# Kernel tuning notes

Measured on AMD Instinct MI355X. Metric: run time of the kernel, lower is better.

## Reference

```python
import jax, jax.numpy as jnp
import numpy as np

# Dims: B=16 graphs, T=354 timesteps (l_max), N=64 nodes, H=128 model dim, NS=32 complex SSM modes

def setup_inputs() -> dict:
    key = jax.random.key(0)
    ks = jax.random.split(key, 10)
    B, T, N, H, NS = 16, 354, 64, 128, 32
    x = jax.random.normal(ks[0], (B, T, N), jnp.float32)
    W_in = jax.random.normal(ks[1], (H, 1), jnp.float32) * 0.5
    b_in = jnp.zeros((H,), jnp.float32)
    # S4D params: timescales log-uniform in [1e-3, 1e-1], A = -1/2 + i*pi*n (S4D-Lin init)
    log_dt = (jnp.log(0.001) + jax.random.uniform(ks[2], (H,), jnp.float32) * (jnp.log(0.1) - jnp.log(0.001))).astype(jnp.float32)
    A_re = -0.5 * jnp.ones((H, NS), jnp.float32)
    A_im = jnp.broadcast_to(np.pi * jnp.arange(NS, dtype=jnp.float32), (H, NS)).astype(jnp.float32) + 0.0
    C_re = jax.random.normal(ks[3], (H, NS), jnp.float32) * (0.5 ** 0.5)
    C_im = jax.random.normal(ks[4], (H, NS), jnp.float32) * (0.5 ** 0.5)
    D = jax.random.normal(ks[5], (H,), jnp.float32)
    W_out = jax.random.normal(ks[6], (2 * H, H), jnp.float32) * (1.0 / np.sqrt(H))
    b_out = jnp.zeros((2 * H,), jnp.float32)
    W_cls = jax.random.normal(ks[7], (1, H), jnp.float32) * (1.0 / np.sqrt(H))
    b_cls = jnp.zeros((1,), jnp.float32)
    return {"x": x, "W_in": W_in, "b_in": b_in, "log_dt": log_dt, "A_re": A_re, "A_im": A_im,
            "C_re": C_re, "C_im": C_im, "D": D, "W_out": W_out, "b_out": b_out,
            "W_cls": W_cls, "b_cls": b_cls}


def reference(x, W_in, b_in, log_dt, A_re, A_im, C_re, C_im, D, W_out, b_out, W_cls, b_cls):
    B, T, N = x.shape
    H = W_in.shape[0]
    # (B,T,N) -> (B*N, T, 1) per-node scalar series
    u = x.transpose(0, 2, 1).reshape(B * N, T, 1)
    u = u * W_in[:, 0] + b_in            # input_proj: (BN, T, H)
    u = u.transpose(0, 2, 1)             # transposed layout: (BN, H, L)
    # ---- S4D kernel (ZOH discretization, conjugate-pair 2*Re trick) ----
    dt = jnp.exp(log_dt)                 # (H,)
    A = A_re + 1j * A_im                 # (H, NS) complex64
    dtA = A * dt[:, None]                # (H, NS)
    C = C_re + 1j * C_im
    C_disc = C * (jnp.exp(dtA) - 1.0) / A
    l = jnp.arange(T)
    vand = jnp.exp(dtA[:, :, None] * l)  # Vandermonde (H, NS, L)
    K = 2.0 * jnp.real(jnp.einsum('hn,hnl->hl', C_disc, vand))  # (H, L)
    # ---- FFT causal long convolution + skip ----
    n_fft = 2 * T
    yf = jnp.fft.rfft(u, n_fft) * jnp.fft.rfft(K, n_fft)
    y = jnp.fft.irfft(yf, n_fft)[..., :T] + D[:, None] * u   # (BN, H, L)
    y = jax.nn.gelu(y)
    # dropout: identity at inference
    # ---- position-wise output linear H -> 2H, then GLU over channels ----
    g = jnp.einsum('bhl,gh->bgl', y, W_out) + b_out[:, None]  # (BN, 2H, L)
    z = g[:, :H] * jax.nn.sigmoid(g[:, H:])                    # (BN, H, L)
    # ---- pooling + classifier ----
    node_feats = z.mean(axis=-1).reshape(B, N, H)
    graph_feats = node_feats.mean(axis=1)                      # (B, H)
    logits = graph_feats @ W_cls.T + b_cls                     # (B, 1)
    return logits
```

## Files before the change

kernel.cpp:

```cpp
#include <hip/hip_runtime.h>
#include <hip/hip_bf16.h>


#define B_  16
#define T_  354
#define N_  64
#define H_  128
#define NS_ 32
#define BN_ (B_*N_)
#define TP_ 384
#define KW_ 512
#define TC_ 23

typedef __attribute__((ext_vector_type(8))) short bf16x8;
typedef __attribute__((ext_vector_type(4))) float f32x4;

static __device__ __forceinline__ unsigned short f32_to_bf16(float f) {
    unsigned int u = __float_as_uint(f);
    unsigned int r = 0x7FFFu + ((u >> 16) & 1u);
    return (unsigned short)((u + r) >> 16);
}

__global__ void k_wprep(const float* __restrict__ W_out, unsigned short* __restrict__ Wbf) {
    int i = blockIdx.x * blockDim.x + threadIdx.x;
    if (i < 2 * H_ * H_) Wbf[i] = f32_to_bf16(W_out[i]);
}

__global__ void k_xprep(const float* __restrict__ x, unsigned short* __restrict__ xbf) {
    int id = blockIdx.x * blockDim.x + threadIdx.x;
    if (id >= T_ * BN_) return;
    int t  = id >> 10;
    int bn = id & 1023;
    float v = x[(bn >> 6) * (T_ * N_) + t * N_ + (bn & 63)];
    xbf[bn * TP_ + t] = f32_to_bf16(v);
}

__global__ __launch_bounds__(512) void k_kern(
        const float* __restrict__ log_dt,
        const float* __restrict__ A_re, const float* __restrict__ A_im,
        const float* __restrict__ C_re, const float* __restrict__ C_im,
        const float* __restrict__ b_in, const float* __restrict__ D,
        unsigned short* __restrict__ Krev, float* __restrict__ koff) {
    const int h = blockIdx.x;
    const int l = threadIdx.x;

    float val = 0.0f;
    if (l < T_) {
        float dt = expf(log_dt[h]);
        float fl = (float)l;
#pragma unroll 4
        for (int m = 0; m < NS_; m++) {
            float are = A_re[h * NS_ + m], aim = A_im[h * NS_ + m];
            float dre = are * dt, dim = aim * dt;
            float er  = expf(dre);
            float c1, s1; __sincosf(dim, &s1, &c1);
            float e_re = er * c1, e_im = er * s1;
            float m_re = e_re - 1.0f, m_im = e_im;
            float inv  = 1.0f / (are * are + aim * aim);
            float q_re = (m_re * are + m_im * aim) * inv;
            float q_im = (m_im * are - m_re * aim) * inv;
            float c_r = C_re[h * NS_ + m], c_i = C_im[h * NS_ + m];
            float cdre = c_r * q_re - c_i * q_im;
            float cdim = c_r * q_im + c_i * q_re;
            float el = expf(dre * fl);
            float cl, sl; __sincosf(dim * fl, &sl, &cl);
            val += el * (cdre * cl - cdim * sl);
        }
        val *= 2.0f;
        if (l == 0) val += D[h];
    }

    __shared__ float sc[512];
    sc[l] = (l < T_) ? val : 0.0f;
    __syncthreads();
    for (int off = 1; off < 512; off <<= 1) {
        float add = (l >= off) ? sc[l - off] : 0.0f;
        __syncthreads();
        sc[l] += add;
        __syncthreads();
    }

    if (l < T_) {
        koff[l * H_ + h] = b_in[h] * sc[l];
        unsigned short bv = f32_to_bf16(val);
#pragma unroll
        for (int r = 0; r < 8; r++)
            Krev[((size_t)r * H_ + h) * KW_ + (T_ - 1 - l) + r] = bv;
    }
}

__global__ __launch_bounds__(256, 2) void k_conv(
        const unsigned short* __restrict__ xbf,
        const unsigned short* __restrict__ Krev,
        const float* __restrict__ koff,
        const float* __restrict__ W_in,
        unsigned short* __restrict__ Y) {
    const int tid  = threadIdx.x;
    const int w    = tid >> 6;
    const int lane = tid & 63;
    const int quad = lane >> 4;
    const int l16  = lane & 15;
    const int bn0  = blockIdx.x * 128;
    const int t    = blockIdx.y;
    const int h0   = w * 32;
    const int nkb  = (t >> 7) + 1;

    f32x4 acc[8][2];
#pragma unroll
    for (int mt = 0; mt < 8; mt++)
#pragma unroll
        for (int nt = 0; nt < 2; nt++) acc[mt][nt] = (f32x4){0.f, 0.f, 0.f, 0.f};

    for (int kb = 0; kb < nkb; kb++) {
        const int tau0 = kb << 7;
        const int s    = (T_ - 1) - t + tau0;
        const int r    = (-s) & 7;
        const unsigned short* bb = Krev + (size_t)r * H_ * KW_ + (s + r);

#pragma unroll
        for (int ks = 0; ks < 4; ks++) {
            bf16x8 bfr[2];
#pragma unroll
            for (int nt = 0; nt < 2; nt++)
                bfr[nt] = *(const bf16x8*)(bb + (h0 + nt * 16 + l16) * KW_
                                           + ks * 32 + quad * 8);
#pragma unroll
            for (int mt = 0; mt < 8; mt++) {
                bf16x8 afr = *(const bf16x8*)(xbf + (size_t)(bn0 + mt * 16 + l16) * TP_
                                              + tau0 + ks * 32 + quad * 8);
                acc[mt][0] = __builtin_amdgcn_mfma_f32_16x16x32_bf16(afr, bfr[0], acc[mt][0], 0, 0, 0);
                acc[mt][1] = __builtin_amdgcn_mfma_f32_16x16x32_bf16(afr, bfr[1], acc[mt][1], 0, 0, 0);
            }
        }
    }

    float win[2], ko[2];
#pragma unroll
    for (int nt = 0; nt < 2; nt++) {
        int h = h0 + nt * 16 + l16;
        win[nt] = W_in[h];
        ko[nt]  = koff[t * H_ + h];
    }

#pragma unroll
    for (int mt = 0; mt < 8; mt++)
#pragma unroll
        for (int nt = 0; nt < 2; nt++)
#pragma unroll
            for (int rr = 0; rr < 4; rr++) {
                float v = fmaf(acc[mt][nt][rr], win[nt], ko[nt]);
                float a  = 0.7978845608028654f * fmaf(0.044715f, v * v * v, v);
                float e  = __expf(2.0f * a);
                float th = 1.0f - 2.0f / (e + 1.0f);
                float g  = 0.5f * v * (1.0f + th);
                int bn = bn0 + mt * 16 + quad * 4 + rr;
                int h  = h0 + nt * 16 + l16;
                Y[((size_t)t * BN_ + bn) * H_ + h] = f32_to_bf16(g);
            }
}

__global__ __launch_bounds__(256, 2) void k_glu(
        const unsigned short* __restrict__ Ybf,
        const unsigned short* __restrict__ Wbf,
        const float* __restrict__ b_out,
        float* __restrict__ node_sum) {
    __shared__ unsigned short W_lds[128 * 136];

    const int tid  = threadIdx.x;
    const int w    = tid >> 6;
    const int lane = tid & 63;
    const int quad = lane >> 4;
    const int l16  = lane & 15;
    const int bn0  = blockIdx.x * 32;
    const int t0   = blockIdx.y * TC_;

    bf16x8 bfrag[4][4];

    for (int p = 0; p < 2; p++) {
        __syncthreads();
#pragma unroll
        for (int it = 0; it < 16; it++) {
            int c  = it * 256 + tid;
            int r  = c >> 5;
            int k4 = (c & 31) * 4;
            uint2 v = *(const uint2*)(Wbf + (size_t)(p * 128 + r) * 128 + k4);
            *(uint2*)&W_lds[r * 136 + k4] = v;
        }
        __syncthreads();
#pragma unroll
        for (int nt = 0; nt < 2; nt++) {
            int r = 32 * w + 16 * nt + l16;
#pragma unroll
            for (int ks = 0; ks < 4; ks++)
                bfrag[p * 2 + nt][ks] = *(const bf16x8*)&W_lds[r * 136 + ks * 32 + quad * 8];
        }
    }

    float bo1[2], bo2[2];
#pragma unroll
    for (int p = 0; p < 2; p++) {
        bo1[p] = b_out[32 * w + 16 * p + l16];
        bo2[p] = b_out[128 + 32 * w + 16 * p + l16];
    }

    f32x4 zacc[2][2];
#pragma unroll
    for (int mt = 0; mt < 2; mt++)
#pragma unroll
        for (int p = 0; p < 2; p++) zacc[mt][p] = (f32x4){0.f, 0.f, 0.f, 0.f};

    for (int tt = 0; tt < TC_; tt++) {
        int t = t0 + tt;
        if (t >= T_) break;
        const unsigned short* yrow = Ybf + (size_t)(t * BN_ + bn0) * H_;

        bf16x8 afrag[2][4];
#pragma unroll
        for (int mt = 0; mt < 2; mt++)
#pragma unroll
            for (int ks = 0; ks < 4; ks++)
                afrag[mt][ks] = *(const bf16x8*)(yrow + (size_t)(16 * mt + l16) * H_
                                                 + ks * 32 + quad * 8);

        f32x4 acc[2][4];
#pragma unroll
        for (int mt = 0; mt < 2; mt++)
#pragma unroll
            for (int nt = 0; nt < 4; nt++) acc[mt][nt] = (f32x4){0.f, 0.f, 0.f, 0.f};

#pragma unroll
        for (int ks = 0; ks < 4; ks++)
#pragma unroll
            for (int nt = 0; nt < 4; nt++)
#pragma unroll
                for (int mt = 0; mt < 2; mt++)
                    acc[mt][nt] = __builtin_amdgcn_mfma_f32_16x16x32_bf16(
                        afrag[mt][ks], bfrag[nt][ks], acc[mt][nt], 0, 0, 0);

#pragma unroll
        for (int mt = 0; mt < 2; mt++)
#pragma unroll
            for (int p = 0; p < 2; p++)
#pragma unroll
                for (int r = 0; r < 4; r++) {
                    float a  = acc[mt][p][r] + bo1[p];
                    float bs = acc[mt][p + 2][r] + bo2[p];
                    float sg = 1.0f / (1.0f + __expf(-bs));
                    zacc[mt][p][r] += a * sg;
                }
    }

#pragma unroll
    for (int mt = 0; mt < 2; mt++)
#pragma unroll
        for (int p = 0; p < 2; p++)
#pragma unroll
            for (int r = 0; r < 4; r++) {
                int bn = bn0 + 16 * mt + quad * 4 + r;
                int j  = 32 * w + 16 * p + l16;
                atomicAdd(&node_sum[bn * H_ + j], zacc[mt][p][r]);
            }
}

__global__ void k_cls(const float* __restrict__ node_sum,
                      const float* __restrict__ W_cls, const float* __restrict__ b_cls,
                      float* __restrict__ out) {
    const int b = blockIdx.x, tid = threadIdx.x;
    float s = 0.0f;
    for (int i = tid; i < N_ * H_; i += 256)
        s += node_sum[b * (N_ * H_) + i] * W_cls[i & (H_ - 1)];
    __shared__ float red[256];
    red[tid] = s;
    __syncthreads();
    for (int off = 128; off > 0; off >>= 1) {
        if (tid < off) red[tid] += red[tid + off];
        __syncthreads();
    }
    if (tid == 0) out[b] = red[0] * (1.0f / (354.0f * 64.0f)) + b_cls[0];
}

extern "C" void kernel_launch(void* const* d_in, const int* in_sizes, int n_in,
                              void* d_out, int out_size, void* d_ws, size_t ws_size,
                              hipStream_t stream) {
    const float* x      = (const float*)d_in[0];
    const float* W_in   = (const float*)d_in[1];
    const float* b_in   = (const float*)d_in[2];
    const float* log_dt = (const float*)d_in[3];
    const float* A_re   = (const float*)d_in[4];
    const float* A_im   = (const float*)d_in[5];
    const float* C_re   = (const float*)d_in[6];
    const float* C_im   = (const float*)d_in[7];
    const float* D      = (const float*)d_in[8];
    const float* W_out  = (const float*)d_in[9];
    const float* b_out  = (const float*)d_in[10];
    const float* W_cls  = (const float*)d_in[11];
    const float* b_cls  = (const float*)d_in[12];

    float* ws = (float*)d_ws;
    float*          node_sum = ws;
    float*          koff     = ws + 131072;
    unsigned short* Wbf      = (unsigned short*)(ws + 176384);
    unsigned short* xbf      = (unsigned short*)(ws + 192768);
    unsigned short* Krev     = (unsigned short*)(ws + 389376);
    unsigned short* Y        = (unsigned short*)(ws + 651520);

    hipMemsetAsync(node_sum, 0, (size_t)BN_ * H_ * sizeof(float), stream);
    hipMemsetAsync(xbf,  0, (size_t)BN_ * TP_ * 2, stream);
    hipMemsetAsync(Krev, 0, (size_t)8 * H_ * KW_ * 2, stream);

    k_wprep<<<dim3(2 * H_ * H_ / 256), dim3(256), 0, stream>>>(W_out, Wbf);
    k_xprep<<<dim3((T_ * BN_ + 255) / 256), dim3(256), 0, stream>>>(x, xbf);
    k_kern<<<dim3(H_), dim3(512), 0, stream>>>(
        log_dt, A_re, A_im, C_re, C_im, b_in, D, Krev, koff);
    k_conv<<<dim3(BN_ / 128, T_), dim3(256), 0, stream>>>(xbf, Krev, koff, W_in, Y);
    k_glu<<<dim3(BN_ / 32, (T_ + TC_ - 1) / TC_), dim3(256), 0, stream>>>(
        Y, Wbf, b_out, node_sum);
    k_cls<<<dim3(B_), dim3(256), 0, stream>>>(node_sum, W_cls, b_cls, (float*)d_out);
}
```

Baseline: 281.4 us.

## Retile causal conv as per-channel Toeplitz GEMM with LDS staging

The convolution kernel is restructured so each block handles one channel h and a 128x128 tile of (node, time). It stages the input rows and the shifted Toeplitz rows of the kernel into LDS with global_load_lds, then runs 4x4 MFMA tiles per wave, replacing the per-timestep grid that reloaded kernel fragments straight from global memory. The GLU kernel now stages each Y timestep tile through LDS, and its time chunk drops from 23 to 6 steps, which gives more blocks. The two prep kernels and the three memsets are merged into one kernel and one memset. In exchange, Y stores become strided by h, with one channel per lane, so write coalescing may get worse.

```diff
diff --git a/kernel.cpp b/kernel.cpp
--- a/kernel.cpp
+++ b/kernel.cpp
@@ -8,9 +8,10 @@
 #define H_  128
 #define NS_ 32
 #define BN_ (B_*N_)
+#define M_  (T_*BN_)
 #define TP_ 384
 #define KW_ 512
-#define TC_ 23
+#define TC_ 6
 
 typedef __attribute__((ext_vector_type(8))) short bf16x8;
 typedef __attribute__((ext_vector_type(4))) float f32x4;
@@ -21,18 +22,24 @@
     return (unsigned short)((u + r) >> 16);
 }
 
-__global__ void k_wprep(const float* __restrict__ W_out, unsigned short* __restrict__ Wbf) {
-    int i = blockIdx.x * blockDim.x + threadIdx.x;
-    if (i < 2 * H_ * H_) Wbf[i] = f32_to_bf16(W_out[i]);
-}
-
-__global__ void k_xprep(const float* __restrict__ x, unsigned short* __restrict__ xbf) {
+static __device__ __forceinline__ void gload_lds4(const void* g, void* l) {
+    __builtin_amdgcn_global_load_lds(
+        (const __attribute__((address_space(1))) unsigned int*)g,
+        (__attribute__((address_space(3))) unsigned int*)l, 4, 0, 0);
+}
+
+__global__ void k_prep(const float* __restrict__ x, const float* __restrict__ W_out,
+                       unsigned short* __restrict__ xbf, unsigned short* __restrict__ Wbf) {
     int id = blockIdx.x * blockDim.x + threadIdx.x;
-    if (id >= T_ * BN_) return;
-    int t  = id >> 10;
-    int bn = id & 1023;
-    float v = x[(bn >> 6) * (T_ * N_) + t * N_ + (bn & 63)];
-    xbf[bn * TP_ + t] = f32_to_bf16(v);
+    if (id < T_ * BN_) {
+        int t  = id >> 10;
+        int bn = id & 1023;
+        float v = x[(bn >> 6) * (T_ * N_) + t * N_ + (bn & 63)];
+        xbf[bn * TP_ + t] = f32_to_bf16(v);
+    } else {
+        int i = id - T_ * BN_;
+        if (i < 2 * H_ * H_) Wbf[i] = f32_to_bf16(W_out[i]);
+    }
 }
 
 __global__ __launch_bounds__(512) void k_kern(
@@ -95,68 +102,88 @@
         const float* __restrict__ koff,
         const float* __restrict__ W_in,
         unsigned short* __restrict__ Y) {
+    __shared__ unsigned short A_lds[128 * 136];
+    __shared__ unsigned short B_lds[128 * 136];
+
     const int tid  = threadIdx.x;
     const int w    = tid >> 6;
     const int lane = tid & 63;
     const int quad = lane >> 4;
     const int l16  = lane & 15;
-    const int bn0  = blockIdx.x * 128;
-    const int t    = blockIdx.y;
-    const int h0   = w * 32;
-    const int nkb  = (t >> 7) + 1;
-
-    f32x4 acc[8][2];
-#pragma unroll
-    for (int mt = 0; mt < 8; mt++)
-#pragma unroll
-        for (int nt = 0; nt < 2; nt++) acc[mt][nt] = (f32x4){0.f, 0.f, 0.f, 0.f};
+    const int h    = blockIdx.x;
+    const int bn0  = blockIdx.y * 128;
+    const int t0   = blockIdx.z * 128;
+    const int wm   = (w & 1) * 64;
+    const int wn   = (w >> 1) * 64;
+    const int nkb  = (t0 >> 7) + 1;
+
+    f32x4 acc[4][4];
+#pragma unroll
+    for (int mt = 0; mt < 4; mt++)
+#pragma unroll
+        for (int nt = 0; nt < 4; nt++) acc[mt][nt] = (f32x4){0.f, 0.f, 0.f, 0.f};
+
+    const unsigned short* krow = Krev + (size_t)h * KW_;
 
     for (int kb = 0; kb < nkb; kb++) {
         const int tau0 = kb << 7;
-        const int s    = (T_ - 1) - t + tau0;
-        const int r    = (-s) & 7;
-        const unsigned short* bb = Krev + (size_t)r * H_ * KW_ + (s + r);
+        __syncthreads();
+#pragma unroll 8
+        for (int i = 0; i < 32; i++) {
+            int r = w * 32 + i;
+            gload_lds4(xbf + (size_t)(bn0 + r) * TP_ + tau0 + lane * 2,
+                       &A_lds[r * 136]);
+        }
+#pragma unroll 8
+        for (int i = 0; i < 32; i++) {
+            int r = w * 32 + i;
+            int L = 353 - (t0 + r) + tau0;
+            if (L < 0) L = 0;
+            int cp = (-L) & 7;
+            gload_lds4(krow + (size_t)cp * H_ * KW_ + L + cp + lane * 2,
+                       &B_lds[r * 136]);
+        }
+        __syncthreads();
 
 #pragma unroll
         for (int ks = 0; ks < 4; ks++) {
-            bf16x8 bfr[2];
-#pragma unroll
-            for (int nt = 0; nt < 2; nt++)
-                bfr[nt] = *(const bf16x8*)(bb + (h0 + nt * 16 + l16) * KW_
-                                           + ks * 32 + quad * 8);
-#pragma unroll
-            for (int mt = 0; mt < 8; mt++) {
-                bf16x8 afr = *(const bf16x8*)(xbf + (size_t)(bn0 + mt * 16 + l16) * TP_
-                                              + tau0 + ks * 32 + quad * 8);
-                acc[mt][0] = __builtin_amdgcn_mfma_f32_16x16x32_bf16(afr, bfr[0], acc[mt][0], 0, 0, 0);
-                acc[mt][1] = __builtin_amdgcn_mfma_f32_16x16x32_bf16(afr, bfr[1], acc[mt][1], 0, 0, 0);
-            }
-        }
-    }
-
-    float win[2], ko[2];
-#pragma unroll
-    for (int nt = 0; nt < 2; nt++) {
-        int h = h0 + nt * 16 + l16;
-        win[nt] = W_in[h];
-        ko[nt]  = koff[t * H_ + h];
-    }
-
-#pragma unroll
-    for (int mt = 0; mt < 8; mt++)
-#pragma unroll
-        for (int nt = 0; nt < 2; nt++)
+            bf16x8 af[4], bfr[4];
+#pragma unroll
+            for (int mt = 0; mt < 4; mt++)
+                af[mt] = *(const bf16x8*)&A_lds[(wm + mt * 16 + l16) * 136 + ks * 32 + quad * 8];
+#pragma unroll
+            for (int nt = 0; nt < 4; nt++)
+                bfr[nt] = *(const bf16x8*)&B_lds[(wn + nt * 16 + l16) * 136 + ks * 32 + quad * 8];
+#pragma unroll
+            for (int nt = 0; nt < 4; nt++)
+#pragma unroll
+                for (int mt = 0; mt < 4; mt++)
+                    acc[mt][nt] = __builtin_amdgcn_mfma_f32_16x16x32_bf16(
+                        af[mt], bfr[nt], acc[mt][nt], 0, 0, 0);
+        }
+    }
+
+    const float win = W_in[h];
+#pragma unroll
+    for (int nt = 0; nt < 4; nt++) {
+        int t = t0 + wn + nt * 16 + l16;
+        bool ok  = (t < T_);
+        float ko = ok ? koff[t * H_ + h] : 0.0f;
+#pragma unroll
+        for (int mt = 0; mt < 4; mt++)
 #pragma unroll
             for (int rr = 0; rr < 4; rr++) {
-                float v = fmaf(acc[mt][nt][rr], win[nt], ko[nt]);
+                float v = fmaf(acc[mt][nt][rr], win, ko);
                 float a  = 0.7978845608028654f * fmaf(0.044715f, v * v * v, v);
                 float e  = __expf(2.0f * a);
                 float th = 1.0f - 2.0f / (e + 1.0f);
                 float g  = 0.5f * v * (1.0f + th);
-                int bn = bn0 + mt * 16 + quad * 4 + rr;
-                int h  = h0 + nt * 16 + l16;
-                Y[((size_t)t * BN_ + bn) * H_ + h] = f32_to_bf16(g);
+                if (ok) {
+                    int bn = bn0 + wm + mt * 16 + quad * 4 + rr;
+                    Y[((size_t)t * BN_ + bn) * H_ + h] = f32_to_bf16(g);
+                }
             }
+    }
 }
 
 __global__ __launch_bounds__(256, 2) void k_glu(
@@ -165,6 +192,7 @@
         const float* __restrict__ b_out,
         float* __restrict__ node_sum) {
     __shared__ unsigned short W_lds[128 * 136];
+    __shared__ unsigned short Yt[32 * 136];
 
     const int tid  = threadIdx.x;
     const int w    = tid >> 6;
@@ -212,15 +240,21 @@
     for (int tt = 0; tt < TC_; tt++) {
         int t = t0 + tt;
         if (t >= T_) break;
-        const unsigned short* yrow = Ybf + (size_t)(t * BN_ + bn0) * H_;
+        __syncthreads();
+#pragma unroll
+        for (int i = 0; i < 8; i++) {
+            int r = w * 8 + i;
+            gload_lds4(Ybf + ((size_t)t * BN_ + bn0 + r) * H_ + lane * 2,
+                       &Yt[r * 136]);
+        }
+        __syncthreads();
 
         bf16x8 afrag[2][4];
 #pragma unroll
         for (int mt = 0; mt < 2; mt++)
 #pragma unroll
             for (int ks = 0; ks < 4; ks++)
-                afrag[mt][ks] = *(const bf16x8*)(yrow + (size_t)(16 * mt + l16) * H_
-                                                 + ks * 32 + quad * 8);
+                afrag[mt][ks] = *(const bf16x8*)&Yt[(mt * 16 + l16) * 136 + ks * 32 + quad * 8];
 
         f32x4 acc[2][4];
 #pragma unroll
@@ -296,23 +330,20 @@
     const float* W_cls  = (const float*)d_in[11];
     const float* b_cls  = (const float*)d_in[12];
 
-    float* ws = (float*)d_ws;
-    float*          node_sum = ws;
-    float*          koff     = ws + 131072;
-    unsigned short* Wbf      = (unsigned short*)(ws + 176384);
-    unsigned short* xbf      = (unsigned short*)(ws + 192768);
-    unsigned short* Krev     = (unsigned short*)(ws + 389376);
-    unsigned short* Y        = (unsigned short*)(ws + 651520);
-
-    hipMemsetAsync(node_sum, 0, (size_t)BN_ * H_ * sizeof(float), stream);
-    hipMemsetAsync(xbf,  0, (size_t)BN_ * TP_ * 2, stream);
-    hipMemsetAsync(Krev, 0, (size_t)8 * H_ * KW_ * 2, stream);
-
-    k_wprep<<<dim3(2 * H_ * H_ / 256), dim3(256), 0, stream>>>(W_out, Wbf);
-    k_xprep<<<dim3((T_ * BN_ + 255) / 256), dim3(256), 0, stream>>>(x, xbf);
+    char* ws = (char*)d_ws;
+    float*          node_sum = (float*)(ws + 0);
+    unsigned short* xbf      = (unsigned short*)(ws + 524288);
+    unsigned short* Krev     = (unsigned short*)(ws + 1310720);
+    float*          koff     = (float*)(ws + 2359296);
+    unsigned short* Wbf      = (unsigned short*)(ws + 2540544);
+    unsigned short* Y        = (unsigned short*)(ws + 2606080);
+
+    hipMemsetAsync(ws, 0, 2359296, stream);
+    k_prep<<<dim3((T_ * BN_ + 2 * H_ * H_ + 255) / 256), dim3(256), 0, stream>>>(
+        x, W_out, xbf, Wbf);
     k_kern<<<dim3(H_), dim3(512), 0, stream>>>(
         log_dt, A_re, A_im, C_re, C_im, b_in, D, Krev, koff);
-    k_conv<<<dim3(BN_ / 128, T_), dim3(256), 0, stream>>>(xbf, Krev, koff, W_in, Y);
+    k_conv<<<dim3(H_, BN_ / 128, 3), dim3(256), 0, stream>>>(xbf, Krev, koff, W_in, Y);
     k_glu<<<dim3(BN_ / 32, (T_ + TC_ - 1) / TC_), dim3(256), 0, stream>>>(
         Y, Wbf, b_out, node_sum);
     k_cls<<<dim3(B_), dim3(256), 0, stream>>>(node_sum, W_cls, b_cls, (float*)d_out);
```

Result: slower. 544.9 us (+93.7%).
